# Performance work log

Measured on AMD Instinct MI355X. Metric: run time of the kernel, lower is better.

Reference implementation:

```python
import jax, jax.numpy as jnp
import numpy as np

ATT = 128  # attention_size
D = 128    # entity_embedding_dim


def setup_inputs() -> dict:
    key = jax.random.key(0)
    k1, k2, k3, k4, k5 = jax.random.split(key, 5)
    B, N, K = 1024, 50, 5
    entity_embedding = jax.random.normal(k1, (B, N, D), dtype=jnp.float32)
    neigh_entity_embedding = jax.random.normal(k2, (B, N, K, D), dtype=jnp.float32)
    neigh_relation_embedding = jax.random.normal(k3, (B, N, K, D), dtype=jnp.float32)
    # fc1: Linear(3*D -> ATT), fc2: Linear(ATT -> 1)
    lim1 = 1.0 / np.sqrt(3 * D)
    lim2 = 1.0 / np.sqrt(ATT)
    W1 = jax.random.uniform(k4, (3 * D, ATT), minval=-lim1, maxval=lim1, dtype=jnp.float32)
    b1 = jnp.zeros((ATT,), dtype=jnp.float32)
    W2 = jax.random.uniform(k5, (ATT, 1), minval=-lim2, maxval=lim2, dtype=jnp.float32)
    b2 = jnp.zeros((1,), dtype=jnp.float32)
    return {
        "entity_embedding": entity_embedding,
        "neigh_entity_embedding": neigh_entity_embedding,
        "neigh_relation_embedding": neigh_relation_embedding,
        "W1": W1, "b1": b1, "W2": W2, "b2": b2,
    }


def reference(entity_embedding, neigh_entity_embedding, neigh_relation_embedding, W1, b1, W2, b2):
    B, N, K, Dd = neigh_entity_embedding.shape
    # expand entity to each of the K neighbors: [B, N, K, D]
    ent_exp = jnp.broadcast_to(entity_embedding[:, :, None, :], (B, N, K, Dd))
    # concat along feature dim -> [B, N, K, 3D]
    concat = jnp.concatenate([ent_exp, neigh_entity_embedding, neigh_relation_embedding], axis=3)
    # tiny MLP: fc1 -> fc2 gives one logit per neighbor
    h = jnp.einsum('bnkf,fa->bnka', concat, W1) + b1          # [B, N, K, ATT]
    logits = jnp.einsum('bnka,ao->bnko', h, W2) + b2          # [B, N, K, 1]
    att = jax.nn.softmax(logits, axis=2)                      # softmax over K neighbors
    neigh_att = jnp.sum(att * neigh_entity_embedding, axis=2) # [B, N, D]
    # squeeze() on [B,N,D] with no singleton dims is identity
    return jnp.concatenate([entity_embedding, neigh_att], axis=-1)  # [B, N, 2D]
```

## Files before the change

### kernel.cpp

```cpp
#include <hip/hip_runtime.h>
#include <math.h>


#define DIM 128
#define KN 5

__global__ void kgat_prep(const float* __restrict__ W1,
                          const float* __restrict__ b1,
                          const float* __restrict__ W2,
                          const float* __restrict__ b2,
                          float* __restrict__ ws) {
    int t = threadIdx.x;
    if (t < 3 * DIM) {
        float s = 0.f;
        #pragma unroll 8
        for (int a = 0; a < DIM; ++a) s += W1[t * DIM + a] * W2[a];
        ws[t] = s;
    }
    if (t == 0) {
        float c = b2[0];
        for (int a = 0; a < DIM; ++a) c += b1[a] * W2[a];
        ws[3 * DIM] = c;
    }
}

__global__ __launch_bounds__(256) void kgat_main(
    const float* __restrict__ ent,
    const float* __restrict__ ne,
    const float* __restrict__ nr,
    const float* __restrict__ ws,
    float* __restrict__ out,
    int P)
{
    const int wave = threadIdx.x >> 6;
    const int lane = threadIdx.x & 63;
    const int p = blockIdx.x * 4 + wave;
    if (p >= P) return;

    const int d2 = 2 * lane;
    const float2 we  = *(const float2*)(ws + d2);
    const float2 wne = *(const float2*)(ws + DIM + d2);
    const float2 wnr = *(const float2*)(ws + 2 * DIM + d2);
    const float  c   = ws[3 * DIM];

    const size_t rowE = (size_t)p * DIM + d2;
    const size_t rowK = ((size_t)p * KN) * DIM + d2;

    const float2 e2 = *(const float2*)(ent + rowE);
    float2 ne2[KN], nr2[KN];
    #pragma unroll
    for (int k = 0; k < KN; ++k) {
        ne2[k] = *(const float2*)(ne + rowK + (size_t)k * DIM);
        nr2[k] = *(const float2*)(nr + rowK + (size_t)k * DIM);
    }

    float red[KN + 1];
    red[0] = e2.x * we.x + e2.y * we.y;
    #pragma unroll
    for (int k = 0; k < KN; ++k)
        red[k + 1] = ne2[k].x * wne.x + ne2[k].y * wne.y
                   + nr2[k].x * wnr.x + nr2[k].y * wnr.y;

    #pragma unroll
    for (int j = 0; j < KN + 1; ++j) {
        float v = red[j];
        #pragma unroll
        for (int off = 32; off >= 1; off >>= 1)
            v += __shfl_xor(v, off, 64);
        red[j] = v;
    }

    float logit[KN];
    float m = -INFINITY;
    #pragma unroll
    for (int k = 0; k < KN; ++k) {
        logit[k] = red[k + 1] + red[0] + c;
        m = fmaxf(m, logit[k]);
    }
    float ex[KN], s = 0.f;
    #pragma unroll
    for (int k = 0; k < KN; ++k) { ex[k] = __expf(logit[k] - m); s += ex[k]; }
    const float inv = 1.f / s;

    float2 acc = {0.f, 0.f};
    #pragma unroll
    for (int k = 0; k < KN; ++k) {
        const float a = ex[k] * inv;
        acc.x += a * ne2[k].x;
        acc.y += a * ne2[k].y;
    }

    float* orow = out + (size_t)p * (2 * DIM);
    *(float2*)(orow + d2) = e2;
    *(float2*)(orow + DIM + d2) = acc;
}

extern "C" void kernel_launch(void* const* d_in, const int* in_sizes, int n_in,
                              void* d_out, int out_size, void* d_ws, size_t ws_size,
                              hipStream_t stream) {
    const float* ent = (const float*)d_in[0];
    const float* ne  = (const float*)d_in[1];
    const float* nr  = (const float*)d_in[2];
    const float* W1  = (const float*)d_in[3];
    const float* b1  = (const float*)d_in[4];
    const float* W2  = (const float*)d_in[5];
    const float* b2  = (const float*)d_in[6];
    float* out = (float*)d_out;
    float* ws  = (float*)d_ws;

    const int P = in_sizes[0] / DIM;

    kgat_prep<<<1, 384, 0, stream>>>(W1, b1, W2, b2, ws);
    const int blocks = (P + 3) / 4;
    kgat_main<<<blocks, 256, 0, stream>>>(ent, ne, nr, ws, out, P);
}
```

Before: 319.6 us.

## Use float4 loads with half-wave per row, parallelize prep, nontemporal stores

The main kernel now gives each half-wave one (b,n) row, so every lane loads 16 bytes instead of 8 and each block covers 8 rows instead of 4. The reduction shortens to five shuffle steps. The prep kernel, which folds W1 and W2, now runs as many waves across several blocks, each doing a coalesced dot product, instead of one thread per output walking a strided row. Output stores become nontemporal to avoid polluting the cache, at the cost of more registers per lane.

```diff
diff --git a/kernel.cpp b/kernel.cpp
--- a/kernel.cpp
+++ b/kernel.cpp
@@ -5,22 +5,36 @@
 #define DIM 128
 #define KN 5
 
-__global__ void kgat_prep(const float* __restrict__ W1,
-                          const float* __restrict__ b1,
-                          const float* __restrict__ W2,
-                          const float* __restrict__ b2,
-                          float* __restrict__ ws) {
-    int t = threadIdx.x;
-    if (t < 3 * DIM) {
-        float s = 0.f;
-        #pragma unroll 8
-        for (int a = 0; a < DIM; ++a) s += W1[t * DIM + a] * W2[a];
-        ws[t] = s;
-    }
-    if (t == 0) {
-        float c = b2[0];
-        for (int a = 0; a < DIM; ++a) c += b1[a] * W2[a];
-        ws[3 * DIM] = c;
+typedef float nfloat4 __attribute__((ext_vector_type(4)));
+
+__device__ __forceinline__ float dot4(nfloat4 a, nfloat4 b) {
+    return a.x * b.x + a.y * b.y + a.z * b.z + a.w * b.w;
+}
+
+__global__ __launch_bounds__(256) void kgat_prep(
+    const float* __restrict__ W1,
+    const float* __restrict__ b1,
+    const float* __restrict__ W2,
+    const float* __restrict__ b2,
+    float* __restrict__ ws)
+{
+    const int gw = blockIdx.x * 4 + (threadIdx.x >> 6);
+    const int lane = threadIdx.x & 63;
+    if (gw < 3 * DIM) {
+        const int t = gw;
+        const float2 w1 = *(const float2*)(W1 + (size_t)t * DIM + 2 * lane);
+        const float2 w2 = *(const float2*)(W2 + 2 * lane);
+        float v = w1.x * w2.x + w1.y * w2.y;
+        #pragma unroll
+        for (int off = 32; off >= 1; off >>= 1) v += __shfl_xor(v, off, 64);
+        if (lane == 0) ws[t] = v;
+    } else if (gw == 3 * DIM) {
+        const float2 bb = *(const float2*)(b1 + 2 * lane);
+        const float2 w2 = *(const float2*)(W2 + 2 * lane);
+        float v = bb.x * w2.x + bb.y * w2.y;
+        #pragma unroll
+        for (int off = 32; off >= 1; off >>= 1) v += __shfl_xor(v, off, 64);
+        if (lane == 0) ws[3 * DIM] = v + b2[0];
     }
 }
 
@@ -34,39 +48,37 @@
 {
     const int wave = threadIdx.x >> 6;
     const int lane = threadIdx.x & 63;
-    const int p = blockIdx.x * 4 + wave;
+    const int half = lane >> 5;
+    const int l    = lane & 31;
+    const int p = blockIdx.x * 8 + wave * 2 + half;
     if (p >= P) return;
 
-    const int d2 = 2 * lane;
-    const float2 we  = *(const float2*)(ws + d2);
-    const float2 wne = *(const float2*)(ws + DIM + d2);
-    const float2 wnr = *(const float2*)(ws + 2 * DIM + d2);
-    const float  c   = ws[3 * DIM];
+    const int d = l * 4;
+    const nfloat4 we  = *(const nfloat4*)(ws + d);
+    const nfloat4 wne = *(const nfloat4*)(ws + DIM + d);
+    const nfloat4 wnr = *(const nfloat4*)(ws + 2 * DIM + d);
+    const float   c   = ws[3 * DIM];
 
-    const size_t rowE = (size_t)p * DIM + d2;
-    const size_t rowK = ((size_t)p * KN) * DIM + d2;
-
-    const float2 e2 = *(const float2*)(ent + rowE);
-    float2 ne2[KN], nr2[KN];
+    const nfloat4 e4 = *(const nfloat4*)(ent + (size_t)p * DIM + d);
+    const size_t rowK = ((size_t)p * KN) * DIM + d;
+    nfloat4 ne4[KN], nr4[KN];
     #pragma unroll
     for (int k = 0; k < KN; ++k) {
-        ne2[k] = *(const float2*)(ne + rowK + (size_t)k * DIM);
-        nr2[k] = *(const float2*)(nr + rowK + (size_t)k * DIM);
+        ne4[k] = *(const nfloat4*)(ne + rowK + (size_t)k * DIM);
+        nr4[k] = *(const nfloat4*)(nr + rowK + (size_t)k * DIM);
     }
 
     float red[KN + 1];
-    red[0] = e2.x * we.x + e2.y * we.y;
+    red[0] = dot4(e4, we);
     #pragma unroll
     for (int k = 0; k < KN; ++k)
-        red[k + 1] = ne2[k].x * wne.x + ne2[k].y * wne.y
-                   + nr2[k].x * wnr.x + nr2[k].y * wnr.y;
+        red[k + 1] = dot4(ne4[k], wne) + dot4(nr4[k], wnr);
 
     #pragma unroll
     for (int j = 0; j < KN + 1; ++j) {
         float v = red[j];
         #pragma unroll
-        for (int off = 32; off >= 1; off >>= 1)
-            v += __shfl_xor(v, off, 64);
+        for (int off = 16; off >= 1; off >>= 1) v += __shfl_xor(v, off, 64);
         red[j] = v;
     }
 
@@ -82,17 +94,19 @@
     for (int k = 0; k < KN; ++k) { ex[k] = __expf(logit[k] - m); s += ex[k]; }
     const float inv = 1.f / s;
 
-    float2 acc = {0.f, 0.f};
+    nfloat4 acc = {0.f, 0.f, 0.f, 0.f};
     #pragma unroll
     for (int k = 0; k < KN; ++k) {
         const float a = ex[k] * inv;
-        acc.x += a * ne2[k].x;
-        acc.y += a * ne2[k].y;
+        acc.x += a * ne4[k].x;
+        acc.y += a * ne4[k].y;
+        acc.z += a * ne4[k].z;
+        acc.w += a * ne4[k].w;
     }
 
     float* orow = out + (size_t)p * (2 * DIM);
-    *(float2*)(orow + d2) = e2;
-    *(float2*)(orow + DIM + d2) = acc;
+    __builtin_nontemporal_store(e4,  (nfloat4*)(orow + d));
+    __builtin_nontemporal_store(acc, (nfloat4*)(orow + DIM + d));
 }
 
 extern "C" void kernel_launch(void* const* d_in, const int* in_sizes, int n_in,
@@ -110,7 +124,6 @@
 
     const int P = in_sizes[0] / DIM;
 
-    kgat_prep<<<1, 384, 0, stream>>>(W1, b1, W2, b2, ws);
-    const int blocks = (P + 3) / 4;
-    kgat_main<<<blocks, 256, 0, stream>>>(ent, ne, nr, ws, out, P);
+    kgat_prep<<<(3 * DIM + 1 + 3) / 4, 256, 0, stream>>>(W1, b1, W2, b2, ws);
+    kgat_main<<<(P + 7) / 8, 256, 0, stream>>>(ent, ne, nr, ws, out, P);
 }
```

Result: faster. 313.1 us (-2.0%).
